# Optimization experiments

Hardware: AMD Instinct MI355X
Metric: run time of the kernel (lower is better)

## Reference

```python
import jax, jax.numpy as jnp
import numpy as np

N = 8192      # total nodes
BG = 8        # graphs in batch
NPG = 1024    # nodes per graph
DEG = 8       # in-degree per node
E = N * DEG   # edges
Q = 16        # queries per graph
D = 768       # in_dim
H = 4         # heads
F = 768       # h_feats per head
HD = H * F    # 3072


def setup_inputs() -> dict:
    key = jax.random.key(0)
    ks = jax.random.split(key, 24)
    x = jax.random.normal(ks[0], (N, D), jnp.float32)
    # block-diagonal random graph: every node has DEG incoming edges from its own graph
    edge_dst = jnp.repeat(jnp.arange(N), DEG)
    edge_src = (edge_dst // NPG) * NPG + jax.random.randint(ks[1], (E,), 0, NPG)
    query_embedding = jax.random.normal(ks[2], (BG, Q, D), jnp.float32) * 0.02
    bert_score = jax.random.uniform(ks[3], (BG, Q, NPG), jnp.float32)

    def lin(k, i, o):
        return jax.random.normal(k, (i, o), jnp.float32) * (1.0 / np.sqrt(i))

    inp = dict(x=x, edge_src=edge_src, edge_dst=edge_dst,
               query_embedding=query_embedding, bert_score=bert_score)
    inp['W1'] = lin(ks[4], D, HD)
    inp['attn_l1'] = jax.random.normal(ks[5], (H, F), jnp.float32) * 0.1
    inp['attn_r1'] = jax.random.normal(ks[6], (H, F), jnp.float32) * 0.1
    inp['b1'] = jax.random.normal(ks[7], (HD,), jnp.float32) * 0.02
    inp['gamma1'] = 1.0 + 0.1 * jax.random.normal(ks[8], (HD,), jnp.float32)
    inp['beta1'] = 0.1 * jax.random.normal(ks[9], (HD,), jnp.float32)
    inp['prelu1'] = 0.25 + 0.01 * jax.random.normal(ks[10], (HD,), jnp.float32)
    inp['W2'] = lin(ks[11], HD, HD)
    inp['attn_l2'] = jax.random.normal(ks[12], (H, F), jnp.float32) * 0.1
    inp['attn_r2'] = jax.random.normal(ks[13], (H, F), jnp.float32) * 0.1
    inp['b2'] = jax.random.normal(ks[14], (HD,), jnp.float32) * 0.02
    inp['gamma2'] = 1.0 + 0.1 * jax.random.normal(ks[15], (HD,), jnp.float32)
    inp['beta2'] = 0.1 * jax.random.normal(ks[16], (HD,), jnp.float32)
    inp['prelu2'] = 0.25 + 0.01 * jax.random.normal(ks[17], (HD,), jnp.float32)
    return inp


def _gat_layer(h, src, dst, W, al, ar, b, gamma, beta, pa):
    # DGL GATConv (eval mode, no residual): fc -> edge attention -> segment softmax -> scatter-sum
    feat = (h @ W).reshape(N, H, F)
    el = jnp.einsum('nhf,hf->nh', feat, al)            # [N,H]
    er = jnp.einsum('nhf,hf->nh', feat, ar)
    e = el[src] + er[dst]                              # [E,H]
    e = jnp.where(e > 0, e, 0.2 * e)                   # leaky_relu(0.2)
    m = jax.ops.segment_max(e, dst, num_segments=N)
    a = jnp.exp(e - m[dst])
    denom = jax.ops.segment_sum(a, dst, num_segments=N)
    alpha = a / denom[dst]                             # edge softmax over in-edges
    rst = jax.ops.segment_sum(feat[src] * alpha[:, :, None], dst, num_segments=N)
    hflat = (rst + b.reshape(1, H, F)).reshape(N, HD)
    # BatchNorm1d (training-mode batch statistics, biased var)
    mu = hflat.mean(axis=0)
    var = hflat.var(axis=0)
    hn = (hflat - mu) * jax.lax.rsqrt(var + 1e-5) * gamma + beta
    # PReLU (per-channel)
    return jnp.where(hn > 0, hn, pa * hn)


def _lambda_mrr(y_pred, y_true):
    # y_pred/y_true: [Q,K]; no padding in this pipeline (y_true = 1/rank > 0)
    order = jnp.argsort(-y_pred, axis=-1)
    yp = jnp.take_along_axis(y_pred, order, axis=-1)
    yt = jnp.take_along_axis(y_true, order, axis=-1)
    mask = (yt[:, :, None] - yt[:, None, :] > 0).astype(yp.dtype)
    sdiff = jnp.clip(yp[:, :, None] - yp[:, None, :], -50.0, 50.0)
    losses = jnp.log1p(jnp.exp(-sdiff))
    return (losses * mask).sum() / mask.sum()


def _forward(x, edge_src, edge_dst, query_embedding, bert_score,
             W1, attn_l1, attn_r1, b1, gamma1, beta1, prelu1,
             W2, attn_l2, attn_r2, b2, gamma2, beta2, prelu2):
    h1 = _gat_layer(x, edge_src, edge_dst, W1, attn_l1, attn_r1, b1, gamma1, beta1, prelu1)
    m1 = h1.reshape(N, H, F).mean(axis=1)
    h2 = _gat_layer(h1, edge_src, edge_dst, W2, attn_l2, attn_r2, b2, gamma2, beta2, prelu2)
    m2 = h2.reshape(N, H, F).mean(axis=1)
    node_rep = jnp.maximum(m1, m2)                      # JumpingKnowledge(max)

    reps = node_rep.reshape(BG, NPG, F)                 # per-graph reps
    reps_flat = node_rep                                # [N,F]
    graph_of = jnp.repeat(jnp.arange(BG), NPG)          # [N]
    rank_gt = (1.0 / jnp.arange(1, NPG + 1, dtype=jnp.float32))[None, :]  # [1,K]

    def per_graph(i, rep_i, q, bs):
        order = jnp.argsort(-bs, axis=-1)               # [Q,NPG] bert rank (desc)
        p = rep_i[order[:, 0]]                          # [Q,F] positive
        neg = rep_i[order[:, 1:]]                       # [Q,NPG-1,F] own negatives
        p_sim = jnp.sum(q * p, axis=-1, keepdims=True)  # [Q,1]
        own_sim = jnp.einsum('qf,qkf->qk', q, neg)      # [Q,NPG-1]
        all_sim = q @ reps_flat.T                       # [Q,N] for in-batch negatives
        other = (graph_of != i).astype(q.dtype)         # mask out own graph
        rank_pred = jnp.concatenate([p_sim, own_sim], axis=-1)  # first K cols of ranking_list
        mrr = _lambda_mrr(rank_pred, jnp.broadcast_to(rank_gt, rank_pred.shape))
        pe = jnp.exp(p_sim).sum(axis=-1)
        ne = jnp.exp(own_sim).sum(axis=-1) + (jnp.exp(all_sim) * other).sum(axis=-1)
        cl = jnp.mean(-jnp.log(pe / (pe + ne)))
        logp = jax.nn.log_softmax(q @ rep_i.T, axis=-1)
        ent = jnp.mean(-(jnp.exp(logp) * logp).sum(axis=-1))
        return cl, mrr, ent

    cl_g, mrr_g, ent_g = jax.vmap(per_graph)(jnp.arange(BG), reps, query_embedding, bert_score)
    return cl_g.mean(), mrr_g.mean(), ent_g.mean()


def reference(x, edge_src, edge_dst, query_embedding, bert_score,
              W1, attn_l1, attn_r1, b1, gamma1, beta1, prelu1,
              W2, attn_l2, attn_r2, b2, gamma2, beta2, prelu2):
    return _forward(x, edge_src, edge_dst, query_embedding, bert_score,
                    W1, attn_l1, attn_r1, b1, gamma1, beta1, prelu1,
                    W2, attn_l2, attn_r2, b2, gamma2, beta2, prelu2)
```

## Files before the change

### kernel.cpp

```cpp
#include <hip/hip_runtime.h>
#include <hip/hip_bf16.h>
#include <hip/hip_fp16.h>

#define NN 8192
#define DD 768
#define HH 4
#define FF 768
#define HD 3072
#define BGr 8
#define NPGr 1024
#define QQ 16
#define NQ 128
#define DEGr 8
#define MRR_TILES 36
#define WSCALE 32.0f
#define WSCALE_INV 0.03125f

typedef __attribute__((ext_vector_type(8))) short bf16x8;
typedef __attribute__((ext_vector_type(4))) float f32x4;
typedef __attribute__((ext_vector_type(2))) float f32x2;
typedef __attribute__((ext_vector_type(4))) int i32x4;
typedef __attribute__((ext_vector_type(8))) int i32x8;

#if defined(__has_builtin)
#  if __has_builtin(__builtin_amdgcn_cvt_pk_fp8_f32) && __has_builtin(__builtin_amdgcn_cvt_pk_f32_fp8)
#    define HW_FP8 1
#  endif
#endif

__device__ __forceinline__ unsigned short f2bf(float f) {
    union { float f; unsigned u; } v; v.f = f;
    unsigned u = v.u;
    unsigned r = (u + 0x7fffu + ((u >> 16) & 1u)) >> 16;
    return (unsigned short)r;
}
__device__ __forceinline__ float bf2f(unsigned short u) {
    union { unsigned u; float f; } v; v.u = ((unsigned)u) << 16;
    return v.f;
}
__device__ __forceinline__ unsigned char f2fp8(float x) {
    unsigned s = (__float_as_uint(x) >> 24) & 0x80;
    __half h = __float2half(fabsf(x) * 0.00390625f);
    unsigned t = (unsigned)__half_as_ushort(h);
    t += 0x3F + ((t >> 7) & 1);
    unsigned b = t >> 7;
    if (b > 0x7E) b = 0x7E;
    return (unsigned char)(s | b);
}
__device__ __forceinline__ float fp82f(unsigned u) {
    unsigned short hb = (unsigned short)(((u & 0x80) << 8) | ((u & 0x7F) << 7));
    return __half2float(__ushort_as_half(hb)) * 256.f;
}
__device__ __forceinline__ unsigned char f2fp8_s(float x) {
#ifdef HW_FP8
    return (unsigned char)(__builtin_amdgcn_cvt_pk_fp8_f32(x, x, 0, false) & 0xFF);
#else
    return f2fp8(x);
#endif
}
__device__ __forceinline__ unsigned f2fp8x4(float a, float b, float c, float d) {
#ifdef HW_FP8
    int lo = __builtin_amdgcn_cvt_pk_fp8_f32(a, b, 0, false);
    int full = __builtin_amdgcn_cvt_pk_fp8_f32(c, d, lo, true);
    return (unsigned)full;
#else
    return (unsigned)f2fp8(a) | ((unsigned)f2fp8(b) << 8) |
           ((unsigned)f2fp8(c) << 16) | ((unsigned)f2fp8(d) << 24);
#endif
}

__device__ __forceinline__ void gl_lds16(const void* g, void* l) {
    __builtin_amdgcn_global_load_lds(
        (const __attribute__((address_space(1))) unsigned int*)g,
        (__attribute__((address_space(3))) unsigned int*)l, 16, 0, 0);
}

#define PB_Z 13
#define PB_CX (PB_Z + 6144)
#define PB_CQ (PB_CX + 96)
#define PB_T1 (PB_CQ + 2304)
#define PB_T2 (PB_T1 + 9216)
__global__ __launch_bounds__(256) void prep_k(const float* __restrict__ x,
                                              unsigned char* __restrict__ xb,
                                              const float* __restrict__ qe,
                                              unsigned short* __restrict__ qeb,
                                              const float* __restrict__ W1,
                                              unsigned char* __restrict__ w1t,
                                              const float* __restrict__ W2,
                                              unsigned char* __restrict__ w2t,
                                              float* __restrict__ stats1,
                                              float* __restrict__ stats2,
                                              float* __restrict__ out) {
    __shared__ float tile[32][33];
    int blk = blockIdx.x, tid = threadIdx.x;
    if (blk < PB_Z) {
        int f = blk * 1024 + tid * 4;
        if (f < 2 * HD) *(float4*)&stats1[f] = make_float4(0.f, 0.f, 0.f, 0.f);
        else if (f < 4 * HD) *(float4*)&stats2[f - 2 * HD] = make_float4(0.f, 0.f, 0.f, 0.f);
        else if (f == 4 * HD) { out[0] = 0.f; out[1] = 0.f; out[2] = 0.f; }
    } else if (blk < PB_CX) {
        int i = (blk - PB_Z) * 256 + tid;
        float4 v = ((const float4*)x)[i];
        ((unsigned*)xb)[i] = f2fp8x4(v.x, v.y, v.z, v.w);
    } else if (blk < PB_CQ) {
        int i = (blk - PB_CX) * 256 + tid;
        float4 v = ((const float4*)qe)[i];
        ushort4 o;
        o.x = f2bf(v.x); o.y = f2bf(v.y); o.z = f2bf(v.z); o.w = f2bf(v.w);
        ((ushort4*)qeb)[i] = o;
    } else {
        const float* in; unsigned char* outp; int K, t;
        if (blk < PB_T1) { in = W1; outp = w1t; K = DD; t = blk - PB_CQ; }
        else             { in = W2; outp = w2t; K = HD; t = blk - PB_T1; }
        int n0 = (t % 96) * 32, k0 = (t / 96) * 32;
        int tx = tid & 31, ty = tid >> 5;
        #pragma unroll
        for (int i = 0; i < 4; i++) {
            int r = ty + i * 8;
            tile[r][tx] = in[(size_t)(k0 + r) * HD + n0 + tx];
        }
        __syncthreads();
        #pragma unroll
        for (int i = 0; i < 4; i++) {
            int r = ty + i * 8;
            outp[(size_t)(n0 + r) * K + k0 + tx] = f2fp8_s(tile[tx][r] * WSCALE);
        }
    }
}

template <bool EPI>
__global__ __launch_bounds__(128, 1) void gemm_fp8(const unsigned char* __restrict__ A,
                                                   const unsigned char* __restrict__ BT,
                                                   unsigned char* __restrict__ C,
                                                   float* __restrict__ elp,
                                                   float* __restrict__ erp,
                                                   const float* __restrict__ al,
                                                   const float* __restrict__ ar,
                                                   int M, int Nc, int K, float inv_scale) {
    __shared__ __align__(16) unsigned char As[2][128 * 128];
    __shared__ __align__(16) unsigned char Bs[2][128 * 128];
    int tid = threadIdx.x;
    int m0 = blockIdx.x * 128;
    int n0 = blockIdx.y * 128;
    int wc = tid >> 6;
    int lane = tid & 63;
    int lm = lane & 15, lq = lane >> 4;

    f32x4 acc[8][4] = {};

    int srow = tid >> 3, su = tid & 7;
    const unsigned char* Ag0[8];
    const unsigned char* Bg0[8];
    unsigned char* AsW[2][8];
    unsigned char* BsW[2][8];
    #pragma unroll
    for (int s = 0; s < 8; s++) {
        int row = srow + 16 * s;
        int uu = su ^ (row & 7);
        Ag0[s] = A  + (size_t)(m0 + row) * K + uu * 16;
        Bg0[s] = BT + (size_t)(n0 + row) * K + uu * 16;
        #pragma unroll
        for (int b = 0; b < 2; b++) {
            AsW[b][s] = &As[b][row * 128 + su * 16];
            BsW[b][s] = &Bs[b][row * 128 + su * 16];
        }
    }

    int NT = K >> 7;
    #pragma unroll
    for (int s = 0; s < 8; s++) {
        gl_lds16(Ag0[s], AsW[0][s]);
        gl_lds16(Bg0[s], BsW[0][s]);
    }

    for (int kt = 0; kt < NT; ++kt) {
        int cur = kt & 1;
        if (kt + 1 < NT) {
            int kb = (kt + 1) << 7;
            #pragma unroll
            for (int s = 0; s < 8; s++) {
                gl_lds16(Ag0[s] + kb, AsW[cur ^ 1][s]);
                gl_lds16(Bg0[s] + kb, BsW[cur ^ 1][s]);
            }
            asm volatile("s_waitcnt vmcnt(16)" ::: "memory");
        } else {
            asm volatile("s_waitcnt vmcnt(0)" ::: "memory");
        }
        asm volatile("s_barrier" ::: "memory");

        const unsigned char* Ab = &As[cur][0];
        const unsigned char* Bb = &Bs[cur][0];
        i32x8 af[8];
        #pragma unroll
        for (int i = 0; i < 8; i++) {
            int row = i * 16 + lm;
            int sw = (row & 7) << 4;
            i32x4 lo = *(const i32x4*)&Ab[row * 128 + ((lq * 32) ^ sw)];
            i32x4 hi = *(const i32x4*)&Ab[row * 128 + ((lq * 32 + 16) ^ sw)];
            i32x8 v;
            v[0] = lo[0]; v[1] = lo[1]; v[2] = lo[2]; v[3] = lo[3];
            v[4] = hi[0]; v[5] = hi[1]; v[6] = hi[2]; v[7] = hi[3];
            af[i] = v;
        }
        __builtin_amdgcn_s_setprio(1);
        #pragma unroll
        for (int j = 0; j < 4; j++) {
            int row = wc * 64 + j * 16 + lm;
            int sw = (row & 7) << 4;
            i32x4 lo = *(const i32x4*)&Bb[row * 128 + ((lq * 32) ^ sw)];
            i32x4 hi = *(const i32x4*)&Bb[row * 128 + ((lq * 32 + 16) ^ sw)];
            i32x8 bv;
            bv[0] = lo[0]; bv[1] = lo[1]; bv[2] = lo[2]; bv[3] = lo[3];
            bv[4] = hi[0]; bv[5] = hi[1]; bv[6] = hi[2]; bv[7] = hi[3];
            #pragma unroll
            for (int i = 0; i < 8; i++)
                acc[i][j] = __builtin_amdgcn_mfma_scale_f32_16x16x128_f8f6f4(
                    af[i], bv, acc[i][j], 0, 0, 0, 127, 0, 127);
        }
        __builtin_amdgcn_s_setprio(0);
        asm volatile("s_barrier" ::: "memory");
    }

    #pragma unroll
    for (int i = 0; i < 8; i++)
        #pragma unroll
        for (int j = 0; j < 4; j++)
            #pragma unroll
            for (int r = 0; r < 4; r++)
                acc[i][j][r] *= inv_scale;

    #pragma unroll
    for (int i = 0; i < 8; i++) {
        int row = m0 + i * 16 + lq * 4;
        #pragma unroll
        for (int j = 0; j < 4; j++) {
            int col = n0 + wc * 64 + j * 16 + lm;
            #pragma unroll
            for (int r = 0; r < 4; r++)
                C[(size_t)(row + r) * Nc + col] = f2fp8_s(acc[i][j][r]);
        }
    }

    if (EPI) {
        int h = n0 / FF;
        int cb = (n0 % FF) >> 7;
        float alv[4], arv[4];
        #pragma unroll
        for (int j = 0; j < 4; j++) {
            int col = n0 + wc * 64 + j * 16 + lm;
            alv[j] = al[col];
            arv[j] = ar[col];
        }
        #pragma unroll
        for (int i = 0; i < 8; i++) {
            #pragma unroll
            for (int r = 0; r < 4; r++) {
                float se = acc[i][0][r] * alv[0] + acc[i][1][r] * alv[1]
                         + acc[i][2][r] * alv[2] + acc[i][3][r] * alv[3];
                float sr_ = acc[i][0][r] * arv[0] + acc[i][1][r] * arv[1]
                          + acc[i][2][r] * arv[2] + acc[i][3][r] * arv[3];
                #pragma unroll
                for (int mm = 1; mm <= 8; mm <<= 1) {
                    se  += __shfl_xor(se, mm, 64);
                    sr_ += __shfl_xor(sr_, mm, 64);
                }
                if (lm == 0) {
                    int row = m0 + i * 16 + lq * 4 + r;
                    size_t slot = ((size_t)row * HH + h) * 12 + cb * 2 + wc;
                    elp[slot] = se;
                    erp[slot] = sr_;
                }
            }
        }
    }
}

__global__ __launch_bounds__(256) void gemm_bt(const unsigned short* __restrict__ A,
                                               const unsigned short* __restrict__ BT,
                                               float* __restrict__ Ct,
                                               int M, int Nc, int K) {
    __shared__ unsigned short As[128 * 64];
    __shared__ unsigned short Bs[128 * 64];
    int tid = threadIdx.x;
    int m0 = blockIdx.x * 128;
    int n0 = blockIdx.y * 128;
    int w = tid >> 6, lane = tid & 63;
    int wr = w >> 1, wc = w & 1;
    int lm = lane & 15, lq = lane >> 4;

    f32x4 acc[4][4] = {};

    int pc = tid & 7;
    const unsigned short* Ag[4];
    const unsigned short* Bg[4];
    unsigned short* AsW[4];
    unsigned short* BsW[4];
    #pragma unroll
    for (int s = 0; s < 4; s++) {
        int row = (tid >> 3) + 32 * s;
        int lc = pc ^ (row & 7);
        Ag[s]  = A  + (size_t)(m0 + row) * K + lc * 8;
        Bg[s]  = BT + (size_t)(n0 + row) * K + lc * 8;
        AsW[s] = &As[(row * 8 + pc) * 8];
        BsW[s] = &Bs[(row * 8 + pc) * 8];
    }

    for (int k0 = 0; k0 < K; k0 += 64) {
        __syncthreads();
        #pragma unroll
        for (int s = 0; s < 4; s++) {
            gl_lds16(Ag[s], AsW[s]);
            gl_lds16(Bg[s], BsW[s]);
        }
        __syncthreads();

        #pragma unroll
        for (int kk = 0; kk < 2; kk++) {
            bf16x8 af[4], bfr[4];
            #pragma unroll
            for (int i = 0; i < 4; i++) {
                int row = wr * 64 + i * 16 + lm;
                int phys = (kk * 4 + lq) ^ (row & 7);
                af[i] = *(const bf16x8*)&As[row * 64 + phys * 8];
            }
            #pragma unroll
            for (int j = 0; j < 4; j++) {
                int row = wc * 64 + j * 16 + lm;
                int phys = (kk * 4 + lq) ^ (row & 7);
                bfr[j] = *(const bf16x8*)&Bs[row * 64 + phys * 8];
            }
            #pragma unroll
            for (int i = 0; i < 4; i++)
                #pragma unroll
                for (int j = 0; j < 4; j++)
                    acc[i][j] = __builtin_amdgcn_mfma_f32_16x16x32_bf16(af[i], bfr[j], acc[i][j], 0, 0, 0);
        }

        #pragma unroll
        for (int s = 0; s < 4; s++) { Ag[s] += 64; Bg[s] += 64; }
    }

    #pragma unroll
    for (int i = 0; i < 4; i++) {
        int row = m0 + wr * 64 + i * 16 + lq * 4;
        #pragma unroll
        for (int j = 0; j < 4; j++) {
            int col = n0 + wc * 64 + j * 16 + lm;
            float4 o = make_float4(acc[i][j][0], acc[i][j][1], acc[i][j][2], acc[i][j][3]);
            *(float4*)&Ct[(size_t)col * M + row] = o;
        }
    }
}

__global__ __launch_bounds__(384) void aggregate_k(const unsigned char* __restrict__ feat,
                                                   const float* __restrict__ elp,
                                                   const float* __restrict__ erp,
                                                   const int* __restrict__ esrc,
                                                   const float* __restrict__ bias,
                                                   unsigned short* __restrict__ out) {
    int b = blockIdx.x;
    int nbase = (b & 7) * NPGr + (b >> 3) * 8;
    int t = threadIdx.x;
    __shared__ int s_src[8][DEGr];
    __shared__ float s_el[8][DEGr][HH];
    __shared__ float s_er[8][HH];
    __shared__ float s_alpha[8][DEGr][HH];
    if (t < 64) s_src[t >> 3][t & 7] = esrc[(size_t)(nbase + (t >> 3)) * DEGr + (t & 7)];
    __syncthreads();
    if (t < 256) {
        int nd = t >> 5, k = (t >> 2) & 7, h = t & 3;
        const float* pp = &elp[((size_t)s_src[nd][k] * HH + h) * 12];
        float s = 0.f;
        #pragma unroll
        for (int q = 0; q < 12; q++) s += pp[q];
        s_el[nd][k][h] = s;
    }
    if (t < 32) {
        int nd = t >> 2, h = t & 3;
        const float* pp = &erp[((size_t)(nbase + nd) * HH + h) * 12];
        float s = 0.f;
        #pragma unroll
        for (int q = 0; q < 12; q++) s += pp[q];
        s_er[nd][h] = s;
    }
    __syncthreads();
    if (t < 32) {
        int nd = t >> 2, h = t & 3;
        float e[DEGr], m = -1e30f;
        #pragma unroll
        for (int k = 0; k < DEGr; k++) {
            float v = s_el[nd][k][h] + s_er[nd][h];
            v = v > 0.f ? v : 0.2f * v;
            e[k] = v; m = fmaxf(m, v);
        }
        float d = 0.f;
        #pragma unroll
        for (int k = 0; k < DEGr; k++) { e[k] = __expf(e[k] - m); d += e[k]; }
        float inv = 1.0f / d;
        #pragma unroll
        for (int k = 0; k < DEGr; k++) s_alpha[nd][k][h] = e[k] * inv;
    }
    __syncthreads();

    int c8 = t * 8;
    int h = t / 96;
    float4 b0 = *(const float4*)&bias[c8];
    float4 b1 = *(const float4*)&bias[c8 + 4];
    float bb[8] = {b0.x, b0.y, b0.z, b0.w, b1.x, b1.y, b1.z, b1.w};
    #pragma unroll
    for (int nd = 0; nd < 8; nd++) {
        float a[8] = {bb[0], bb[1], bb[2], bb[3], bb[4], bb[5], bb[6], bb[7]};
        #pragma unroll
        for (int k = 0; k < DEGr; k++) {
            float wv = s_alpha[nd][k][h];
            unsigned long fv = *(const unsigned long*)&feat[(size_t)s_src[nd][k] * HD + c8];
#ifdef HW_FP8
            unsigned w0 = (unsigned)fv, w1 = (unsigned)(fv >> 32);
            f32x2 d0 = __builtin_amdgcn_cvt_pk_f32_fp8((int)w0, false);
            f32x2 d1 = __builtin_amdgcn_cvt_pk_f32_fp8((int)w0, true);
            f32x2 d2 = __builtin_amdgcn_cvt_pk_f32_fp8((int)w1, false);
            f32x2 d3 = __builtin_amdgcn_cvt_pk_f32_fp8((int)w1, true);
            a[0] += wv * d0[0]; a[1] += wv * d0[1];
            a[2] += wv * d1[0]; a[3] += wv * d1[1];
            a[4] += wv * d2[0]; a[5] += wv * d2[1];
            a[6] += wv * d3[0]; a[7] += wv * d3[1];
#else
            #pragma unroll
            for (int e = 0; e < 8; e++)
                a[e] += wv * fp82f((unsigned)((fv >> (8 * e)) & 0xFF));
#endif
        }
        union { unsigned short u[8]; bf16x8 v; } o;
        #pragma unroll
        for (int e = 0; e < 8; e++) o.u[e] = f2bf(a[e]);
        *(bf16x8*)&out[(size_t)(nbase + nd) * HD + c8] = o.v;
    }
}

__global__ __launch_bounds__(256) void ln_stats_k(const unsigned short* __restrict__ x,
                                                  float* __restrict__ sums) {
    int col = (blockIdx.x * 256 + threadIdx.x) * 4;
    int r0 = blockIdx.y * 128;
    float s[4] = {0.f, 0.f, 0.f, 0.f}, s2[4] = {0.f, 0.f, 0.f, 0.f};
    for (int r = r0; r < r0 + 128; r++) {
        ushort4 v = *(const ushort4*)&x[(size_t)r * HD + col];
        float f0 = bf2f(v.x), f1 = bf2f(v.y), f2 = bf2f(v.z), f3 = bf2f(v.w);
        s[0] += f0; s[1] += f1; s[2] += f2; s[3] += f3;
        s2[0] += f0 * f0; s2[1] += f1 * f1; s2[2] += f2 * f2; s2[3] += f3 * f3;
    }
    #pragma unroll
    for (int e = 0; e < 4; e++) {
        atomicAdd(&sums[col + e], s[e]);
        atomicAdd(&sums[HD + col + e], s2[e]);
    }
}

__global__ __launch_bounds__(192) void ln_norm_mean_k(const unsigned short* __restrict__ x,
                                                      const float* __restrict__ sums,
                                                      const float* __restrict__ gamma,
                                                      const float* __restrict__ beta,
                                                      const float* __restrict__ prelu,
                                                      unsigned char* __restrict__ h,
                                                      unsigned short* __restrict__ m1) {
    int n0 = blockIdx.x * 8, tid = threadIdx.x;
    int c = tid * 4;
    const float invN = 1.0f / (float)NN;
    float mu_[HH][4], aa_[HH][4], bb_[HH][4], pp_[HH][4];
    #pragma unroll
    for (int hh = 0; hh < HH; hh++) {
        int col = hh * FF + c;
        float4 sm = *(const float4*)&sums[col];
        float4 sq = *(const float4*)&sums[HD + col];
        float4 g = *(const float4*)&gamma[col];
        float4 b = *(const float4*)&beta[col];
        float4 p = *(const float4*)&prelu[col];
        float smv[4] = {sm.x, sm.y, sm.z, sm.w}, sqv[4] = {sq.x, sq.y, sq.z, sq.w};
        float gv[4] = {g.x, g.y, g.z, g.w}, bv[4] = {b.x, b.y, b.z, b.w};
        float pv[4] = {p.x, p.y, p.z, p.w};
        #pragma unroll
        for (int e = 0; e < 4; e++) {
            float mu = smv[e] * invN;
            float var = sqv[e] * invN - mu * mu;
            float rs = rsqrtf(var + 1e-5f);
            mu_[hh][e] = mu; aa_[hh][e] = rs * gv[e];
            bb_[hh][e] = bv[e]; pp_[hh][e] = pv[e];
        }
    }
    for (int nd = 0; nd < 8; nd++) {
        int n = n0 + nd;
        float acc4[4] = {0.f, 0.f, 0.f, 0.f};
        #pragma unroll
        for (int hh = 0; hh < HH; hh++) {
            int col = hh * FF + c;
            ushort4 v = *(const ushort4*)&x[(size_t)n * HD + col];
            float vv[4] = {bf2f(v.x), bf2f(v.y), bf2f(v.z), bf2f(v.w)};
            float val[4];
            #pragma unroll
            for (int e = 0; e < 4; e++) {
                float t = (vv[e] - mu_[hh][e]) * aa_[hh][e] + bb_[hh][e];
                val[e] = t > 0.f ? t : pp_[hh][e] * t;
                acc4[e] += val[e];
            }
            *(unsigned*)&h[(size_t)n * HD + col] = f2fp8x4(val[0], val[1], val[2], val[3]);
        }
        ushort4 o;
        o.x = f2bf(0.25f * acc4[0]); o.y = f2bf(0.25f * acc4[1]);
        o.z = f2bf(0.25f * acc4[2]); o.w = f2bf(0.25f * acc4[3]);
        *(ushort4*)&m1[(size_t)n * FF + c] = o;
    }
}

__global__ __launch_bounds__(192) void ln_norm_rep_k(const unsigned short* __restrict__ x,
                                                     const float* __restrict__ sums,
                                                     const float* __restrict__ gamma,
                                                     const float* __restrict__ beta,
                                                     const float* __restrict__ prelu,
                                                     const unsigned short* __restrict__ m1,
                                                     unsigned short* __restrict__ rep) {
    int n0 = blockIdx.x * 8, tid = threadIdx.x;
    int c = tid * 4;
    const float invN = 1.0f / (float)NN;
    float mu_[HH][4], aa_[HH][4], bb_[HH][4], pp_[HH][4];
    #pragma unroll
    for (int hh = 0; hh < HH; hh++) {
        int col = hh * FF + c;
        float4 sm = *(const float4*)&sums[col];
        float4 sq = *(const float4*)&sums[HD + col];
        float4 g = *(const float4*)&gamma[col];
        float4 b = *(const float4*)&beta[col];
        float4 p = *(const float4*)&prelu[col];
        float smv[4] = {sm.x, sm.y, sm.z, sm.w}, sqv[4] = {sq.x, sq.y, sq.z, sq.w};
        float gv[4] = {g.x, g.y, g.z, g.w}, bv[4] = {b.x, b.y, b.z, b.w};
        float pv[4] = {p.x, p.y, p.z, p.w};
        #pragma unroll
        for (int e = 0; e < 4; e++) {
            float mu = smv[e] * invN;
            float var = sqv[e] * invN - mu * mu;
            float rs = rsqrtf(var + 1e-5f);
            mu_[hh][e] = mu; aa_[hh][e] = rs * gv[e];
            bb_[hh][e] = bv[e]; pp_[hh][e] = pv[e];
        }
    }
    for (int nd = 0; nd < 8; nd++) {
        int n = n0 + nd;
        float acc4[4] = {0.f, 0.f, 0.f, 0.f};
        #pragma unroll
        for (int hh = 0; hh < HH; hh++) {
            int col = hh * FF + c;
            ushort4 v = *(const ushort4*)&x[(size_t)n * HD + col];
            float vv[4] = {bf2f(v.x), bf2f(v.y), bf2f(v.z), bf2f(v.w)};
            #pragma unroll
            for (int e = 0; e < 4; e++) {
                float t = (vv[e] - mu_[hh][e]) * aa_[hh][e] + bb_[hh][e];
                acc4[e] += t > 0.f ? t : pp_[hh][e] * t;
            }
        }
        ushort4 m = *(const ushort4*)&m1[(size_t)n * FF + c];
        ushort4 o;
        o.x = f2bf(fmaxf(bf2f(m.x), 0.25f * acc4[0]));
        o.y = f2bf(fmaxf(bf2f(m.y), 0.25f * acc4[1]));
        o.z = f2bf(fmaxf(bf2f(m.z), 0.25f * acc4[2]));
        o.w = f2bf(fmaxf(bf2f(m.w), 0.25f * acc4[3]));
        *(ushort4*)&rep[(size_t)n * FF + c] = o;
    }
}

__global__ __launch_bounds__(256) void loss_k(const float* __restrict__ simsQ,
                                              const float* __restrict__ bert,
                                              float* __restrict__ out) {
    __shared__ float s_ya[128];
    __shared__ float s_ba[128];
    __shared__ float red[256];
    __shared__ int redi[256];
    int tid = threadIdx.x;

    if (blockIdx.x < NQ * MRR_TILES) {
        int qq = blockIdx.x / MRR_TILES;
        int t36 = blockIdx.x % MRR_TILES;
        int I = 0, rem = t36;
        while (rem >= 8 - I) { rem -= 8 - I; I++; }
        int J = I + rem;
        int g = qq >> 4;
        const float* Y = simsQ + (size_t)qq * NN + (size_t)g * NPGr;
        const float* B = bert + (size_t)qq * NPGr;
        int a0 = I * 128, b0 = J * 128;

        if (tid < 128) s_ya[tid] = Y[a0 + tid];
        else           s_ba[tid - 128] = B[a0 + (tid - 128)];
        int bl = tid & 127;
        int bcol = b0 + bl;
        float yb = Y[bcol];
        float bbv = B[bcol];
        __syncthreads();

        const float L2E = 1.44269504f;
        int abase = (tid >> 7) * 64;
        float s = 0.f;
        if (I == J) {
            #pragma unroll 4
            for (int ai = 0; ai < 64; ai++) {
                int a = abase + ai;
                float ya = s_ya[a], ba = s_ba[a];
                float tdf = ya - yb;
                float d = (bbv > ba) ? tdf : -tdf;
                float xv = fminf(fmaxf(d, -50.f), 50.f);
                float term = __builtin_amdgcn_logf(1.0f + __builtin_amdgcn_exp2f(xv * L2E));
                s += (bl > a) ? term : 0.f;
            }
        } else {
            #pragma unroll 4
            for (int ai = 0; ai < 64; ai++) {
                int a = abase + ai;
                float ya = s_ya[a], ba = s_ba[a];
                float tdf = ya - yb;
                float d = (bbv > ba) ? tdf : -tdf;
                float xv = fminf(fmaxf(d, -50.f), 50.f);
                s += __builtin_amdgcn_logf(1.0f + __builtin_amdgcn_exp2f(xv * L2E));
            }
        }
        red[tid] = s; __syncthreads();
        for (int o = 128; o; o >>= 1) { if (tid < o) red[tid] += red[tid + o]; __syncthreads(); }
        if (tid == 0)
            atomicAdd(&out[1], red[0] * (0.69314718f / (523776.0f * (float)NQ)));
    } else {
        int qq = blockIdx.x - NQ * MRR_TILES;
        int g = qq >> 4;
        const float* S = simsQ + (size_t)qq * NN;
        const float* Sg = S + g * NPGr;
        float m = -1e30f;
        for (int n = tid; n < NN; n += 256) m = fmaxf(m, S[n]);
        red[tid] = m; __syncthreads();
        for (int o = 128; o; o >>= 1) { if (tid < o) red[tid] = fmaxf(red[tid], red[tid + o]); __syncthreads(); }
        float mAll = red[0]; __syncthreads();
        float mg = -1e30f;
        for (int j = tid; j < NPGr; j += 256) mg = fmaxf(mg, Sg[j]);
        red[tid] = mg; __syncthreads();
        for (int o = 128; o; o >>= 1) { if (tid < o) red[tid] = fmaxf(red[tid], red[tid + o]); __syncthreads(); }
        float mG = red[0]; __syncthreads();
        float z = 0.f;
        for (int n = tid; n < NN; n += 256) z += __expf(S[n] - mAll);
        red[tid] = z; __syncthreads();
        for (int o = 128; o; o >>= 1) { if (tid < o) red[tid] += red[tid + o]; __syncthreads(); }
        float Zall = red[0]; __syncthreads();
        float zg = 0.f, tg = 0.f;
        for (int j = tid; j < NPGr; j += 256) {
            float s = Sg[j];
            float e = __expf(s - mG);
            zg += e; tg += e * s;
        }
        red[tid] = zg; __syncthreads();
        for (int o = 128; o; o >>= 1) { if (tid < o) red[tid] += red[tid + o]; __syncthreads(); }
        float Zg = red[0]; __syncthreads();
        red[tid] = tg; __syncthreads();
        for (int o = 128; o; o >>= 1) { if (tid < o) red[tid] += red[tid + o]; __syncthreads(); }
        float Tg = red[0]; __syncthreads();
        float bb = -1e30f; int bi = NPGr;
        for (int j = tid; j < NPGr; j += 256) {
            float v = bert[(size_t)qq * NPGr + j];
            if (v > bb) { bb = v; bi = j; }
        }
        red[tid] = bb; redi[tid] = bi; __syncthreads();
        for (int o = 128; o; o >>= 1) {
            if (tid < o) {
                if (red[tid + o] > red[tid] || (red[tid + o] == red[tid] && redi[tid + o] < redi[tid])) {
                    red[tid] = red[tid + o]; redi[tid] = redi[tid + o];
                }
            }
            __syncthreads();
        }
        if (tid == 0) {
            float p_sim = Sg[redi[0]];
            float lse = mAll + logf(Zall);
            atomicAdd(&out[0], (lse - p_sim) * (1.0f / (float)NQ));
            float entv = (mG + logf(Zg)) - Tg / Zg;
            atomicAdd(&out[2], entv * (1.0f / (float)NQ));
        }
    }
}

extern "C" void kernel_launch(void* const* d_in, const int* in_sizes, int n_in,
                              void* d_out, int out_size, void* d_ws, size_t ws_size,
                              hipStream_t stream) {
    const float* x    = (const float*)d_in[0];
    const int* esrc   = (const int*)d_in[1];
    const float* qe   = (const float*)d_in[3];
    const float* bert = (const float*)d_in[4];
    const float* W1   = (const float*)d_in[5];
    const float* al1  = (const float*)d_in[6];
    const float* ar1  = (const float*)d_in[7];
    const float* b1   = (const float*)d_in[8];
    const float* g1   = (const float*)d_in[9];
    const float* be1  = (const float*)d_in[10];
    const float* p1   = (const float*)d_in[11];
    const float* W2   = (const float*)d_in[12];
    const float* al2  = (const float*)d_in[13];
    const float* ar2  = (const float*)d_in[14];
    const float* b2   = (const float*)d_in[15];
    const float* g2   = (const float*)d_in[16];
    const float* be2  = (const float*)d_in[17];
    const float* p2   = (const float*)d_in[18];
    float* out = (float*)d_out;
    (void)in_sizes; (void)n_in; (void)out_size; (void)ws_size;

    char* p = (char*)d_ws;
    auto alloc = [&](size_t bytes) -> void* {
        void* r = (void*)p;
        p += (bytes + 255) & ~(size_t)255;
        return r;
    };
    unsigned char*  featB = (unsigned char*)alloc((size_t)NN * HD);
    unsigned short* hflat = (unsigned short*)alloc((size_t)NN * HD * 2);
    unsigned char*  hbuf  = (unsigned char*)alloc((size_t)NN * HD);
    unsigned short* repb  = (unsigned short*)alloc((size_t)NN * FF * 2);
    unsigned char*  w1t   = (unsigned char*)alloc((size_t)HD * DD);
    unsigned char*  w2t   = (unsigned char*)alloc((size_t)HD * HD);
    unsigned short* m1    = (unsigned short*)alloc((size_t)NN * FF * 2);
    float* elp            = (float*)alloc((size_t)NN * HH * 12 * 4);
    float* erp            = (float*)alloc((size_t)NN * HH * 12 * 4);
    unsigned short* qeb   = (unsigned short*)alloc((size_t)NQ * FF * 2);
    float* simsQ          = (float*)alloc((size_t)NQ * NN * 4);
    float* stats1         = (float*)alloc((size_t)2 * HD * 4);
    float* stats2         = (float*)alloc((size_t)2 * HD * 4);
    unsigned char* xb     = (unsigned char*)repb;

    prep_k<<<PB_T2, 256, 0, stream>>>(x, xb, qe, qeb, W1, w1t, W2, w2t, stats1, stats2, out);

    gemm_fp8<true><<<dim3(NN / 128, HD / 128), 128, 0, stream>>>(
        xb, w1t, featB, elp, erp, al1, ar1, NN, HD, DD, WSCALE_INV);
    aggregate_k<<<NN / 8, 384, 0, stream>>>(featB, elp, erp, esrc, b1, hflat);
    ln_stats_k<<<dim3(HD / 1024, NN / 128), 256, 0, stream>>>(hflat, stats1);
    ln_norm_mean_k<<<NN / 8, 192, 0, stream>>>(hflat, stats1, g1, be1, p1, hbuf, m1);

    gemm_fp8<true><<<dim3(NN / 128, HD / 128), 128, 0, stream>>>(
        hbuf, w2t, featB, elp, erp, al2, ar2, NN, HD, HD, WSCALE_INV);
    aggregate_k<<<NN / 8, 384, 0, stream>>>(featB, elp, erp, esrc, b2, hflat);
    ln_stats_k<<<dim3(HD / 1024, NN / 128), 256, 0, stream>>>(hflat, stats2);
    ln_norm_rep_k<<<NN / 8, 192, 0, stream>>>(hflat, stats2, g2, be2, p2, m1, repb);

    gemm_bt<<<dim3(NN / 128, 1), 256, 0, stream>>>(repb, qeb, simsQ, NN, NQ, FF);

    loss_k<<<NQ * MRR_TILES + NQ, 256, 0, stream>>>(simsQ, bert, out);
}
```

Measured before the change: 555.2 us.

## Enlarge FP8 GEMM block tile to 256x256 with eight waves

The FP8 GEMM now uses a 256x256 output tile per block with 512 threads arranged as 2x4 waves, in place of 128x128 with 2 waves. Each wave still computes a 128x64 sub-tile, and the staging loads and epilogue slot indexing are remapped to match. The aim is to raise operand reuse from shared memory and cut global traffic per output. In exchange it uses 128KB of LDS per block and launches fewer blocks (384 per GEMM), which may limit occupancy and leave CUs unevenly loaded.

New measurement: 520.5 us. 6.3% less time.

```diff
diff --git a/kernel.cpp b/kernel.cpp
--- a/kernel.cpp
+++ b/kernel.cpp
@@ -129,7 +129,7 @@
 }
 
 template <bool EPI>
-__global__ __launch_bounds__(128, 1) void gemm_fp8(const unsigned char* __restrict__ A,
+__global__ __launch_bounds__(512, 2) void gemm_fp8(const unsigned char* __restrict__ A,
                                                    const unsigned char* __restrict__ BT,
                                                    unsigned char* __restrict__ C,
                                                    float* __restrict__ elp,
@@ -137,40 +137,30 @@
                                                    const float* __restrict__ al,
                                                    const float* __restrict__ ar,
                                                    int M, int Nc, int K, float inv_scale) {
-    __shared__ __align__(16) unsigned char As[2][128 * 128];
-    __shared__ __align__(16) unsigned char Bs[2][128 * 128];
+    __shared__ __align__(16) unsigned char As[2][256 * 128];
+    __shared__ __align__(16) unsigned char Bs[2][256 * 128];
     int tid = threadIdx.x;
-    int m0 = blockIdx.x * 128;
-    int n0 = blockIdx.y * 128;
-    int wc = tid >> 6;
+    int m0 = blockIdx.x * 256;
+    int n0 = blockIdx.y * 256;
+    int w = tid >> 6;
+    int wr = w >> 2;
+    int wq = w & 3;
     int lane = tid & 63;
     int lm = lane & 15, lq = lane >> 4;
 
     f32x4 acc[8][4] = {};
 
     int srow = tid >> 3, su = tid & 7;
-    const unsigned char* Ag0[8];
-    const unsigned char* Bg0[8];
-    unsigned char* AsW[2][8];
-    unsigned char* BsW[2][8];
-    #pragma unroll
-    for (int s = 0; s < 8; s++) {
-        int row = srow + 16 * s;
-        int uu = su ^ (row & 7);
-        Ag0[s] = A  + (size_t)(m0 + row) * K + uu * 16;
-        Bg0[s] = BT + (size_t)(n0 + row) * K + uu * 16;
-        #pragma unroll
-        for (int b = 0; b < 2; b++) {
-            AsW[b][s] = &As[b][row * 128 + su * 16];
-            BsW[b][s] = &Bs[b][row * 128 + su * 16];
-        }
-    }
+    int uu = su ^ (srow & 7);
+    const unsigned char* Ab0 = A  + (size_t)(m0 + srow) * K + uu * 16;
+    const unsigned char* Bb0 = BT + (size_t)(n0 + srow) * K + uu * 16;
+    int asOff = srow * 128 + su * 16;
 
     int NT = K >> 7;
     #pragma unroll
-    for (int s = 0; s < 8; s++) {
-        gl_lds16(Ag0[s], AsW[0][s]);
-        gl_lds16(Bg0[s], BsW[0][s]);
+    for (int s = 0; s < 4; s++) {
+        gl_lds16(Ab0 + (size_t)64 * s * K, &As[0][asOff + s * 8192]);
+        gl_lds16(Bb0 + (size_t)64 * s * K, &Bs[0][asOff + s * 8192]);
     }
 
     for (int kt = 0; kt < NT; ++kt) {
@@ -178,25 +168,25 @@
         if (kt + 1 < NT) {
             int kb = (kt + 1) << 7;
             #pragma unroll
-            for (int s = 0; s < 8; s++) {
-                gl_lds16(Ag0[s] + kb, AsW[cur ^ 1][s]);
-                gl_lds16(Bg0[s] + kb, BsW[cur ^ 1][s]);
-            }
-            asm volatile("s_waitcnt vmcnt(16)" ::: "memory");
+            for (int s = 0; s < 4; s++) {
+                gl_lds16(Ab0 + kb + (size_t)64 * s * K, &As[cur ^ 1][asOff + s * 8192]);
+                gl_lds16(Bb0 + kb + (size_t)64 * s * K, &Bs[cur ^ 1][asOff + s * 8192]);
+            }
+            asm volatile("s_waitcnt vmcnt(8)" ::: "memory");
         } else {
             asm volatile("s_waitcnt vmcnt(0)" ::: "memory");
         }
         asm volatile("s_barrier" ::: "memory");
 
-        const unsigned char* Ab = &As[cur][0];
-        const unsigned char* Bb = &Bs[cur][0];
+        const unsigned char* Abuf = &As[cur][0];
+        const unsigned char* Bbuf = &Bs[cur][0];
         i32x8 af[8];
         #pragma unroll
         for (int i = 0; i < 8; i++) {
-            int row = i * 16 + lm;
+            int row = wr * 128 + i * 16 + lm;
             int sw = (row & 7) << 4;
-            i32x4 lo = *(const i32x4*)&Ab[row * 128 + ((lq * 32) ^ sw)];
-            i32x4 hi = *(const i32x4*)&Ab[row * 128 + ((lq * 32 + 16) ^ sw)];
+            i32x4 lo = *(const i32x4*)&Abuf[row * 128 + ((lq * 32) ^ sw)];
+            i32x4 hi = *(const i32x4*)&Abuf[row * 128 + ((lq * 32 + 16) ^ sw)];
             i32x8 v;
             v[0] = lo[0]; v[1] = lo[1]; v[2] = lo[2]; v[3] = lo[3];
             v[4] = hi[0]; v[5] = hi[1]; v[6] = hi[2]; v[7] = hi[3];
@@ -205,10 +195,10 @@
         __builtin_amdgcn_s_setprio(1);
         #pragma unroll
         for (int j = 0; j < 4; j++) {
-            int row = wc * 64 + j * 16 + lm;
+            int row = wq * 64 + j * 16 + lm;
             int sw = (row & 7) << 4;
-            i32x4 lo = *(const i32x4*)&Bb[row * 128 + ((lq * 32) ^ sw)];
-            i32x4 hi = *(const i32x4*)&Bb[row * 128 + ((lq * 32 + 16) ^ sw)];
+            i32x4 lo = *(const i32x4*)&Bbuf[row * 128 + ((lq * 32) ^ sw)];
+            i32x4 hi = *(const i32x4*)&Bbuf[row * 128 + ((lq * 32 + 16) ^ sw)];
             i32x8 bv;
             bv[0] = lo[0]; bv[1] = lo[1]; bv[2] = lo[2]; bv[3] = lo[3];
             bv[4] = hi[0]; bv[5] = hi[1]; bv[6] = hi[2]; bv[7] = hi[3];
@@ -231,10 +221,10 @@
 
     #pragma unroll
     for (int i = 0; i < 8; i++) {
-        int row = m0 + i * 16 + lq * 4;
+        int row = m0 + wr * 128 + i * 16 + lq * 4;
         #pragma unroll
         for (int j = 0; j < 4; j++) {
-            int col = n0 + wc * 64 + j * 16 + lm;
+            int col = n0 + wq * 64 + j * 16 + lm;
             #pragma unroll
             for (int r = 0; r < 4; r++)
                 C[(size_t)(row + r) * Nc + col] = f2fp8_s(acc[i][j][r]);
@@ -243,11 +233,12 @@
 
     if (EPI) {
         int h = n0 / FF;
-        int cb = (n0 % FF) >> 7;
+        int cb = ((n0 % FF) >> 7) + (wq >> 1);
+        int wc = wq & 1;
         float alv[4], arv[4];
         #pragma unroll
         for (int j = 0; j < 4; j++) {
-            int col = n0 + wc * 64 + j * 16 + lm;
+            int col = n0 + wq * 64 + j * 16 + lm;
             alv[j] = al[col];
             arv[j] = ar[col];
         }
@@ -265,7 +256,7 @@
                     sr_ += __shfl_xor(sr_, mm, 64);
                 }
                 if (lm == 0) {
-                    int row = m0 + i * 16 + lq * 4 + r;
+                    int row = m0 + wr * 128 + i * 16 + lq * 4 + r;
                     size_t slot = ((size_t)row * HH + h) * 12 + cb * 2 + wc;
                     elp[slot] = se;
                     erp[slot] = sr_;
@@ -725,13 +716,13 @@
 
     prep_k<<<PB_T2, 256, 0, stream>>>(x, xb, qe, qeb, W1, w1t, W2, w2t, stats1, stats2, out);
 
-    gemm_fp8<true><<<dim3(NN / 128, HD / 128), 128, 0, stream>>>(
+    gemm_fp8<true><<<dim3(NN / 256, HD / 256), 512, 0, stream>>>(
         xb, w1t, featB, elp, erp, al1, ar1, NN, HD, DD, WSCALE_INV);
     aggregate_k<<<NN / 8, 384, 0, stream>>>(featB, elp, erp, esrc, b1, hflat);
     ln_stats_k<<<dim3(HD / 1024, NN / 128), 256, 0, stream>>>(hflat, stats1);
     ln_norm_mean_k<<<NN / 8, 192, 0, stream>>>(hflat, stats1, g1, be1, p1, hbuf, m1);
 
-    gemm_fp8<true><<<dim3(NN / 128, HD / 128), 128, 0, stream>>>(
+    gemm_fp8<true><<<dim3(NN / 256, HD / 256), 512, 0, stream>>>(
         hbuf, w2t, featB, elp, erp, al2, ar2, NN, HD, HD, WSCALE_INV);
     aggregate_k<<<NN / 8, 384, 0, stream>>>(featB, elp, erp, esrc, b2, hflat);
     ln_stats_k<<<dim3(HD / 1024, NN / 128), 256, 0, stream>>>(hflat, stats2);
```
